# Kernel tuning notes

Hardware: AMD Instinct MI355X
Metric: run time of the kernel (lower is better)

The kernel has to match this reference:

```python
import jax, jax.numpy as jnp
import numpy as np

N, G, K, D = 16, 4096, 8, 2  # agents, grid points (64x64 flattened), fiber dim, manifold dim


def setup_inputs() -> dict:
    key = jax.random.key(0)
    k0, k1, k2, k3 = jax.random.split(key, 4)
    I = jnp.eye(K, dtype=jnp.float32)
    # frames and links: identity + small perturbation (invertible, as init_twist_scale=0.05 implies)
    omega = I + 0.05 * jax.random.normal(k0, (N, G, K, K), dtype=jnp.float32)
    links = I + 0.05 * jax.random.normal(k1, (N, D, G, K, K), dtype=jnp.float32)
    mu_q = jax.random.normal(k2, (N, G, K), dtype=jnp.float32)
    A = 0.3 * jax.random.normal(k3, (N, G, K, K), dtype=jnp.float32)
    sigma_q = A @ A.swapaxes(-1, -2) + I  # SPD covariances
    return {"omega": omega, "links": links, "mu_q": mu_q, "sigma_q": sigma_q}


def reference(omega, links, mu_q, sigma_q):
    """pairwise_alignment_with_twists: E[i,j,g] = KL(q_i || Omega_ij[q_j]).

    full_transport: Omega_ij = omega_i @ V_i @ inv(omega_j),
    V_i = I + sum_d (link_{i,d} - I)   (links depend only on i, per source).
    """
    I = jnp.eye(K, dtype=omega.dtype)
    V = I + jnp.sum(links - I, axis=1)                       # (N,G,K,K)
    T = omega @ V                                            # omega_i V_i, (N,G,K,K)
    omega_inv = jnp.linalg.inv(omega)                        # (N,G,K,K)
    Om = jnp.einsum('igab,jgbc->ijgac', T, omega_inv)        # (N,N,G,K,K)

    mu_t = jnp.einsum('ijgab,jgb->ijga', Om, mu_q)           # transported means
    sig_t = jnp.einsum('ijgab,jgbc,ijgdc->ijgad', Om, sigma_q, Om)  # Om Sigma Om^T

    inv2 = jnp.linalg.inv(sig_t)                             # Sigma2^{-1}
    diff = mu_t - mu_q[:, None]                              # (N,N,G,K)
    tr = jnp.einsum('ijgab,igba->ijg', inv2, sigma_q)        # tr(Sigma2^{-1} Sigma1)
    quad = jnp.einsum('ijga,ijgab,ijgb->ijg', diff, inv2, diff)
    ld2 = jnp.linalg.slogdet(sig_t)[1]                       # (N,N,G)
    ld1 = jnp.linalg.slogdet(sigma_q)[1]                     # (N,G)
    E = 0.5 * (tr + quad - K + ld2 - ld1[:, None, :])
    # zero the diagonal (i == j skipped in the original loop)
    mask = 1.0 - jnp.eye(N, dtype=E.dtype)
    return E * mask[:, :, None]
```

## Files before the change

kernel.cpp:

```cpp
#include <hip/hip_runtime.h>
#include <math.h>

#define NN 16
#define GG 4096
#define GP 2
#define STR 76
#define NWG (GG / GP)

template <int CTRL>
__device__ __forceinline__ float dppf(float x) {
    return __builtin_bit_cast(float, __builtin_amdgcn_mov_dpp(
        __builtin_bit_cast(int, x), CTRL, 0xF, 0xF, true));
}
__device__ __forceinline__ float qb(float x, int L) {
    switch (L) {
        case 0:  return dppf<0x00>(x);
        case 1:  return dppf<0x55>(x);
        case 2:  return dppf<0xAA>(x);
        default: return dppf<0xFF>(x);
    }
}
__device__ __forceinline__ float qsum(float x) {
    x += dppf<0xB1>(x);
    x += dppf<0x4E>(x);
    return x;
}
__device__ __forceinline__ void bcast_row(float out[8], const float r0[8],
                                          const float r1[8], int k) {
#pragma unroll
    for (int c = 0; c < 8; ++c) {
        float s = (k < 4) ? r0[c] : r1[c];
        out[c] = qb(s, k & 3);
    }
}
__device__ __forceinline__ float sel_lo(const float r[8], int q) {
    return (q == 0) ? r[0] : (q == 1) ? r[1] : (q == 2) ? r[2] : r[3];
}
__device__ __forceinline__ float sel_hi(const float r[8], int q) {
    return (q == 0) ? r[4] : (q == 1) ? r[5] : (q == 2) ? r[6] : r[7];
}
__device__ __forceinline__ void ld_row(float r[8], const float* p) {
    float4 x = *(const float4*)p, y = *(const float4*)(p + 4);
    r[0] = x.x; r[1] = x.y; r[2] = x.z; r[3] = x.w;
    r[4] = y.x; r[5] = y.y; r[6] = y.z; r[7] = y.w;
}
__device__ __forceinline__ void st_row(float* p, const float r[8]) {
    *(float4*)p       = make_float4(r[0], r[1], r[2], r[3]);
    *(float4*)(p + 4) = make_float4(r[4], r[5], r[6], r[7]);
}
__device__ __forceinline__ float dot8(const float a[8], const float b[8]) {
    float s = a[0] * b[0];
    s = fmaf(a[1], b[1], s); s = fmaf(a[2], b[2], s);
    s = fmaf(a[3], b[3], s); s = fmaf(a[4], b[4], s);
    s = fmaf(a[5], b[5], s); s = fmaf(a[6], b[6], s);
    s = fmaf(a[7], b[7], s);
    return s;
}

__device__ __forceinline__ float gj4(float r0[8], float r1[8], int q) {
    float pp = 1.0f;
#pragma unroll
    for (int k = 0; k < 8; ++k) {
        float Mk[8];
        bcast_row(Mk, r0, r1, k);
        float p = Mk[k];
        pp *= p;
        float ip = 1.0f / p;
        bool own0 = (k < 4) && (q == k);
        bool own1 = (k >= 4) && (q == k - 4);
        float m0 = -(own0 ? -1.0f : r0[k]) * ip;
        float m1 = -(own1 ? -1.0f : r1[k]) * ip;
#pragma unroll
        for (int c = 0; c < 8; ++c) {
            float b0 = own0 ? 0.0f : r0[c];
            float b1 = own1 ? 0.0f : r1[c];
            r0[c] = fmaf(m0, Mk[c], b0);
            r1[c] = fmaf(m1, Mk[c], b1);
        }
        r0[k] = m0;
        r1[k] = m1;
    }
    return pp;
}

__global__ __launch_bounds__(256) void pairkl_kernel(
    const float* __restrict__ omega, const float* __restrict__ links,
    const float* __restrict__ mu, const float* __restrict__ sigma,
    float* __restrict__ out) {
    __shared__ __align__(16) float sh_x[GP][NN][STR];
    __shared__ __align__(16) float sh_y[GP][NN][STR];

    const int bid  = blockIdx.x;
    const int work = (bid & 7) * (NWG / 8) + (bid >> 3);
    const int g0   = work * GP;
    const int t    = threadIdx.x;
    const int wid  = t >> 6;
    const int gl   = wid & 1;
    const int isB  = wid >> 1;
    const int lane = t & 63;
    const int item = lane >> 2;
    const int q    = lane & 3;
    const int g    = g0 + gl;
    const int mb   = (item * GG + g) * 64;

    if (!isB) {
        float v0[8], v1[8], o0[8], o1[8], s0[8], s1[8], mq[8];
        {
            const float* l0p = links + ((item * 2 + 0) * GG + g) * 64;
            const float* l1p = links + ((item * 2 + 1) * GG + g) * 64;
            float la[8], lb[8];
            ld_row(la, l0p + q * 8);
            ld_row(lb, l1p + q * 8);
#pragma unroll
            for (int c = 0; c < 8; ++c)
                v0[c] = la[c] + lb[c] - ((c == q) ? 1.f : 0.f);
            ld_row(la, l0p + (q + 4) * 8);
            ld_row(lb, l1p + (q + 4) * 8);
#pragma unroll
            for (int c = 0; c < 8; ++c)
                v1[c] = la[c] + lb[c] - ((c == q + 4) ? 1.f : 0.f);
        }
        ld_row(o0, omega + mb + q * 8);
        ld_row(o1, omega + mb + (q + 4) * 8);
        ld_row(s0, sigma + mb + q * 8);
        ld_row(s1, sigma + mb + (q + 4) * 8);
        ld_row(mq, mu + (item * GG + g) * 8);
        float R0[8], R1[8];
#pragma unroll
        for (int c = 0; c < 8; ++c) { R0[c] = 0.f; R1[c] = 0.f; }
#pragma unroll
        for (int b = 0; b < 8; ++b) {
            float Vb[8]; bcast_row(Vb, v0, v1, b);
#pragma unroll
            for (int c = 0; c < 8; ++c) {
                R0[c] = fmaf(o0[b], Vb[c], R0[c]);
                R1[c] = fmaf(o1[b], Vb[c], R1[c]);
            }
        }
        float ldT = logf(fabsf(gj4(R0, R1, q)));
        float Z0[8], Z1[8];
#pragma unroll
        for (int c = 0; c < 8; ++c) { Z0[c] = 0.f; Z1[c] = 0.f; }
#pragma unroll
        for (int b = 0; b < 8; ++b) {
            float Sb[8]; bcast_row(Sb, s0, s1, b);
#pragma unroll
            for (int c = 0; c < 8; ++c) {
                Z0[c] = fmaf(R0[b], Sb[c], Z0[c]);
                Z1[c] = fmaf(R1[b], Sb[c], Z1[c]);
            }
        }
        float u_lo = dot8(R0, mq), u_hi = dot8(R1, mq);
        float uf[8];
#pragma unroll
        for (int c = 0; c < 4; ++c) { uf[c] = qb(u_lo, c); uf[c + 4] = qb(u_hi, c); }
        float X0[8], X1[8];
#pragma unroll
        for (int c = 0; c < 8; ++c) {
            float Wc[8]; bcast_row(Wc, R0, R1, c);
            X0[c] = fmaf(u_lo, uf[c], dot8(Z0, Wc));
            X1[c] = fmaf(u_hi, uf[c], dot8(Z1, Wc));
        }
        st_row(&sh_x[gl][item][q * 8], X0);
        st_row(&sh_x[gl][item][(q + 4) * 8], X1);
        if (q == 0) {
            *(float4*)&sh_x[gl][item][64] = make_float4(uf[0], uf[1], uf[2], uf[3]);
            *(float4*)&sh_x[gl][item][68] = make_float4(uf[4], uf[5], uf[6], uf[7]);
            *(float2*)&sh_x[gl][item][72] = make_float2(2.f * ldT, 1.f);
        }
    } else {
        float o0[8], o1[8], s0[8], s1[8], mq[8];
        ld_row(o0, omega + mb + q * 8);
        ld_row(o1, omega + mb + (q + 4) * 8);
        ld_row(s0, sigma + mb + q * 8);
        ld_row(s1, sigma + mb + (q + 4) * 8);
        ld_row(mq, mu + (item * GG + g) * 8);
        float ld1 = logf(fabsf(gj4(s0, s1, q)));
        float cc  = qsum(dot8(s0, mq) * sel_lo(mq, q) +
                         dot8(s1, mq) * sel_hi(mq, q));
        if (q == 0) *(float2*)&sh_x[gl][item][74] = make_float2(-ld1, 0.f);
        float t10[8], t11[8];
#pragma unroll
        for (int c = 0; c < 8; ++c) { t10[c] = 0.f; t11[c] = 0.f; }
#pragma unroll
        for (int a = 0; a < 8; ++a) {
            float Oa[8]; bcast_row(Oa, o0, o1, a);
            float Sa[8]; bcast_row(Sa, s0, s1, a);
            float oqa = sel_lo(Oa, q), oqa4 = sel_hi(Oa, q);
#pragma unroll
            for (int c = 0; c < 8; ++c) {
                t10[c] = fmaf(oqa,  Sa[c], t10[c]);
                t11[c] = fmaf(oqa4, Sa[c], t11[c]);
            }
        }
        float w_lo = dot8(t10, mq), w_hi = dot8(t11, mq);
        float wf[8];
#pragma unroll
        for (int c = 0; c < 4; ++c) { wf[c] = qb(w_lo, c); wf[c + 4] = qb(w_hi, c); }
        float P0[8], P1[8];
#pragma unroll
        for (int c = 0; c < 8; ++c) { P0[c] = 0.f; P1[c] = 0.f; }
#pragma unroll
        for (int b = 0; b < 8; ++b) {
            float Ob[8]; bcast_row(Ob, o0, o1, b);
#pragma unroll
            for (int c = 0; c < 8; ++c) {
                P0[c] = fmaf(t10[b], Ob[c], P0[c]);
                P1[c] = fmaf(t11[b], Ob[c], P1[c]);
            }
        }
        st_row(&sh_y[gl][item][q * 8], P0);
        st_row(&sh_y[gl][item][(q + 4) * 8], P1);
        float ldo = logf(fabsf(gj4(o0, o1, q)));
        if (q == 0) {
            float s_j = ld1 - 2.f * ldo + cc - 8.0f;
            *(float4*)&sh_y[gl][item][64] =
                make_float4(-2.f * wf[0], -2.f * wf[1], -2.f * wf[2], -2.f * wf[3]);
            *(float4*)&sh_y[gl][item][68] =
                make_float4(-2.f * wf[4], -2.f * wf[5], -2.f * wf[6], -2.f * wf[7]);
            *(float4*)&sh_y[gl][item][72] = make_float4(1.f, s_j, 1.f, 0.f);
        }
    }
    __syncthreads();

    if (t < 128) {
        const int gl2 = t >> 6, r = t & 63;
        const int i0 = r >> 3, j0 = r & 7;
        const int i1 = i0 + 8, j1 = j0 + 8;
        const float4* x0 = (const float4*)&sh_x[gl2][i0][0];
        const float4* x1 = (const float4*)&sh_x[gl2][i1][0];
        const float4* y0 = (const float4*)&sh_y[gl2][j0][0];
        const float4* y1 = (const float4*)&sh_y[gl2][j1][0];
        float d00 = 0.f, d01 = 0.f, d10 = 0.f, d11 = 0.f;
#pragma unroll
        for (int k = 0; k < STR / 4; ++k) {
            float4 a0 = x0[k], a1 = x1[k], b0 = y0[k], b1 = y1[k];
            d00 = fmaf(a0.x, b0.x, d00); d00 = fmaf(a0.y, b0.y, d00);
            d00 = fmaf(a0.z, b0.z, d00); d00 = fmaf(a0.w, b0.w, d00);
            d01 = fmaf(a0.x, b1.x, d01); d01 = fmaf(a0.y, b1.y, d01);
            d01 = fmaf(a0.z, b1.z, d01); d01 = fmaf(a0.w, b1.w, d01);
            d10 = fmaf(a1.x, b0.x, d10); d10 = fmaf(a1.y, b0.y, d10);
            d10 = fmaf(a1.z, b0.z, d10); d10 = fmaf(a1.w, b0.w, d10);
            d11 = fmaf(a1.x, b1.x, d11); d11 = fmaf(a1.y, b1.y, d11);
            d11 = fmaf(a1.z, b1.z, d11); d11 = fmaf(a1.w, b1.w, d11);
        }
        const int gg = g0 + gl2;
        const bool dg = (i0 == j0);
        out[(i0 * NN + j0) * GG + gg] = dg ? 0.f : 0.5f * d00;
        out[(i0 * NN + j1) * GG + gg] = 0.5f * d01;
        out[(i1 * NN + j0) * GG + gg] = 0.5f * d10;
        out[(i1 * NN + j1) * GG + gg] = dg ? 0.f : 0.5f * d11;
    }
}

extern "C" void kernel_launch(void* const* d_in, const int* in_sizes, int n_in,
                              void* d_out, int out_size, void* d_ws, size_t ws_size,
                              hipStream_t stream) {
    const float* omega = (const float*)d_in[0];
    const float* links = (const float*)d_in[1];
    const float* mu    = (const float*)d_in[2];
    const float* sigma = (const float*)d_in[3];
    float* out = (float*)d_out;
    hipLaunchKernelGGL(pairkl_kernel, dim3(NWG), dim3(256), 0, stream,
                       omega, links, mu, sigma, out);
}
```

Before: 26.96 us.

## Collapse to one wave per grid point, removing block barrier

Each grid point is now handled by a single 64-lane wavefront that does both the source-side and target-side work in sequence, instead of four waves split across two grid points and two roles. The __syncthreads is replaced by a compiler memory fence, since LDS exchange stays inside one wave, and the final pairwise dot-product phase uses all lanes instead of half the block. Register arrays are reused to limit pressure. The cost is that each wave now carries twice the serial ALU work and the launch has 4096 small blocks, which cuts per-wave parallelism and adds scheduling overhead.

```diff
diff --git a/kernel.cpp b/kernel.cpp
--- a/kernel.cpp
+++ b/kernel.cpp
@@ -3,9 +3,8 @@
 
 #define NN 16
 #define GG 4096
-#define GP 2
 #define STR 76
-#define NWG (GG / GP)
+#define NWG GG
 
 template <int CTRL>
 __device__ __forceinline__ float dppf(float x) {
@@ -83,48 +82,42 @@
     return pp;
 }
 
-__global__ __launch_bounds__(256) void pairkl_kernel(
+__global__ __launch_bounds__(64) void pairkl_kernel(
     const float* __restrict__ omega, const float* __restrict__ links,
     const float* __restrict__ mu, const float* __restrict__ sigma,
     float* __restrict__ out) {
-    __shared__ __align__(16) float sh_x[GP][NN][STR];
-    __shared__ __align__(16) float sh_y[GP][NN][STR];
+    __shared__ __align__(16) float sh_x[NN][STR];
+    __shared__ __align__(16) float sh_y[NN][STR];
 
     const int bid  = blockIdx.x;
-    const int work = (bid & 7) * (NWG / 8) + (bid >> 3);
-    const int g0   = work * GP;
-    const int t    = threadIdx.x;
-    const int wid  = t >> 6;
-    const int gl   = wid & 1;
-    const int isB  = wid >> 1;
-    const int lane = t & 63;
+    const int g    = (bid & 7) * (NWG / 8) + (bid >> 3);
+    const int lane = threadIdx.x;
     const int item = lane >> 2;
     const int q    = lane & 3;
-    const int g    = g0 + gl;
     const int mb   = (item * GG + g) * 64;
 
-    if (!isB) {
-        float v0[8], v1[8], o0[8], o1[8], s0[8], s1[8], mq[8];
-        {
-            const float* l0p = links + ((item * 2 + 0) * GG + g) * 64;
-            const float* l1p = links + ((item * 2 + 1) * GG + g) * 64;
-            float la[8], lb[8];
-            ld_row(la, l0p + q * 8);
-            ld_row(lb, l1p + q * 8);
-#pragma unroll
-            for (int c = 0; c < 8; ++c)
-                v0[c] = la[c] + lb[c] - ((c == q) ? 1.f : 0.f);
-            ld_row(la, l0p + (q + 4) * 8);
-            ld_row(lb, l1p + (q + 4) * 8);
-#pragma unroll
-            for (int c = 0; c < 8; ++c)
-                v1[c] = la[c] + lb[c] - ((c == q + 4) ? 1.f : 0.f);
-        }
-        ld_row(o0, omega + mb + q * 8);
-        ld_row(o1, omega + mb + (q + 4) * 8);
-        ld_row(s0, sigma + mb + q * 8);
-        ld_row(s1, sigma + mb + (q + 4) * 8);
-        ld_row(mq, mu + (item * GG + g) * 8);
+    float o0[8], o1[8], s0[8], s1[8], v0[8], v1[8], mq[8];
+    {
+        const float* l0p = links + ((item * 2 + 0) * GG + g) * 64;
+        const float* l1p = links + ((item * 2 + 1) * GG + g) * 64;
+        float la[8], lb[8];
+        ld_row(la, l0p + q * 8);
+        ld_row(lb, l1p + q * 8);
+#pragma unroll
+        for (int c = 0; c < 8; ++c) v0[c] = la[c] + lb[c] - ((c == q) ? 1.f : 0.f);
+        ld_row(la, l0p + (q + 4) * 8);
+        ld_row(lb, l1p + (q + 4) * 8);
+#pragma unroll
+        for (int c = 0; c < 8; ++c) v1[c] = la[c] + lb[c] - ((c == q + 4) ? 1.f : 0.f);
+    }
+    ld_row(o0, omega + mb + q * 8);
+    ld_row(o1, omega + mb + (q + 4) * 8);
+    ld_row(s0, sigma + mb + q * 8);
+    ld_row(s1, sigma + mb + (q + 4) * 8);
+    ld_row(mq, mu + (item * GG + g) * 8);
+
+    float ldT, u_lo, u_hi, uf[8];
+    {
         float R0[8], R1[8];
 #pragma unroll
         for (int c = 0; c < 8; ++c) { R0[c] = 0.f; R1[c] = 0.f; }
@@ -137,7 +130,7 @@
                 R1[c] = fmaf(o1[b], Vb[c], R1[c]);
             }
         }
-        float ldT = logf(fabsf(gj4(R0, R1, q)));
+        ldT = logf(fabsf(gj4(R0, R1, q)));
         float Z0[8], Z1[8];
 #pragma unroll
         for (int c = 0; c < 8; ++c) { Z0[c] = 0.f; Z1[c] = 0.f; }
@@ -150,35 +143,24 @@
                 Z1[c] = fmaf(R1[b], Sb[c], Z1[c]);
             }
         }
-        float u_lo = dot8(R0, mq), u_hi = dot8(R1, mq);
-        float uf[8];
+        u_lo = dot8(R0, mq);
+        u_hi = dot8(R1, mq);
 #pragma unroll
         for (int c = 0; c < 4; ++c) { uf[c] = qb(u_lo, c); uf[c + 4] = qb(u_hi, c); }
-        float X0[8], X1[8];
 #pragma unroll
         for (int c = 0; c < 8; ++c) {
             float Wc[8]; bcast_row(Wc, R0, R1, c);
-            X0[c] = fmaf(u_lo, uf[c], dot8(Z0, Wc));
-            X1[c] = fmaf(u_hi, uf[c], dot8(Z1, Wc));
-        }
-        st_row(&sh_x[gl][item][q * 8], X0);
-        st_row(&sh_x[gl][item][(q + 4) * 8], X1);
-        if (q == 0) {
-            *(float4*)&sh_x[gl][item][64] = make_float4(uf[0], uf[1], uf[2], uf[3]);
-            *(float4*)&sh_x[gl][item][68] = make_float4(uf[4], uf[5], uf[6], uf[7]);
-            *(float2*)&sh_x[gl][item][72] = make_float2(2.f * ldT, 1.f);
-        }
-    } else {
-        float o0[8], o1[8], s0[8], s1[8], mq[8];
-        ld_row(o0, omega + mb + q * 8);
-        ld_row(o1, omega + mb + (q + 4) * 8);
-        ld_row(s0, sigma + mb + q * 8);
-        ld_row(s1, sigma + mb + (q + 4) * 8);
-        ld_row(mq, mu + (item * GG + g) * 8);
-        float ld1 = logf(fabsf(gj4(s0, s1, q)));
-        float cc  = qsum(dot8(s0, mq) * sel_lo(mq, q) +
-                         dot8(s1, mq) * sel_hi(mq, q));
-        if (q == 0) *(float2*)&sh_x[gl][item][74] = make_float2(-ld1, 0.f);
+            v0[c] = fmaf(u_lo, uf[c], dot8(Z0, Wc));
+            v1[c] = fmaf(u_hi, uf[c], dot8(Z1, Wc));
+        }
+        st_row(&sh_x[item][q * 8], v0);
+        st_row(&sh_x[item][(q + 4) * 8], v1);
+    }
+
+    float ld1, cc, wf[8];
+    {
+        ld1 = logf(fabsf(gj4(s0, s1, q)));
+        cc  = qsum(dot8(s0, mq) * sel_lo(mq, q) + dot8(s1, mq) * sel_hi(mq, q));
         float t10[8], t11[8];
 #pragma unroll
         for (int c = 0; c < 8; ++c) { t10[c] = 0.f; t11[c] = 0.f; }
@@ -194,43 +176,45 @@
             }
         }
         float w_lo = dot8(t10, mq), w_hi = dot8(t11, mq);
-        float wf[8];
 #pragma unroll
         for (int c = 0; c < 4; ++c) { wf[c] = qb(w_lo, c); wf[c + 4] = qb(w_hi, c); }
-        float P0[8], P1[8];
-#pragma unroll
-        for (int c = 0; c < 8; ++c) { P0[c] = 0.f; P1[c] = 0.f; }
+#pragma unroll
+        for (int c = 0; c < 8; ++c) { s0[c] = 0.f; s1[c] = 0.f; }
 #pragma unroll
         for (int b = 0; b < 8; ++b) {
             float Ob[8]; bcast_row(Ob, o0, o1, b);
 #pragma unroll
             for (int c = 0; c < 8; ++c) {
-                P0[c] = fmaf(t10[b], Ob[c], P0[c]);
-                P1[c] = fmaf(t11[b], Ob[c], P1[c]);
-            }
-        }
-        st_row(&sh_y[gl][item][q * 8], P0);
-        st_row(&sh_y[gl][item][(q + 4) * 8], P1);
-        float ldo = logf(fabsf(gj4(o0, o1, q)));
-        if (q == 0) {
-            float s_j = ld1 - 2.f * ldo + cc - 8.0f;
-            *(float4*)&sh_y[gl][item][64] =
-                make_float4(-2.f * wf[0], -2.f * wf[1], -2.f * wf[2], -2.f * wf[3]);
-            *(float4*)&sh_y[gl][item][68] =
-                make_float4(-2.f * wf[4], -2.f * wf[5], -2.f * wf[6], -2.f * wf[7]);
-            *(float4*)&sh_y[gl][item][72] = make_float4(1.f, s_j, 1.f, 0.f);
-        }
-    }
-    __syncthreads();
-
-    if (t < 128) {
-        const int gl2 = t >> 6, r = t & 63;
-        const int i0 = r >> 3, j0 = r & 7;
+                s0[c] = fmaf(t10[b], Ob[c], s0[c]);
+                s1[c] = fmaf(t11[b], Ob[c], s1[c]);
+            }
+        }
+        st_row(&sh_y[item][q * 8], s0);
+        st_row(&sh_y[item][(q + 4) * 8], s1);
+    }
+    float ldo = logf(fabsf(gj4(o0, o1, q)));
+
+    if (q == 0) {
+        float a_i = 2.f * ldT - ld1;
+        float s_j = ld1 - 2.f * ldo + cc - 8.0f;
+        *(float4*)&sh_x[item][64] = make_float4(uf[0], uf[1], uf[2], uf[3]);
+        *(float4*)&sh_x[item][68] = make_float4(uf[4], uf[5], uf[6], uf[7]);
+        *(float4*)&sh_x[item][72] = make_float4(a_i, 1.f, 0.f, 0.f);
+        *(float4*)&sh_y[item][64] =
+            make_float4(-2.f * wf[0], -2.f * wf[1], -2.f * wf[2], -2.f * wf[3]);
+        *(float4*)&sh_y[item][68] =
+            make_float4(-2.f * wf[4], -2.f * wf[5], -2.f * wf[6], -2.f * wf[7]);
+        *(float4*)&sh_y[item][72] = make_float4(1.f, s_j, 0.f, 0.f);
+    }
+    asm volatile("" ::: "memory");
+
+    {
+        const int i0 = lane >> 3, j0 = lane & 7;
         const int i1 = i0 + 8, j1 = j0 + 8;
-        const float4* x0 = (const float4*)&sh_x[gl2][i0][0];
-        const float4* x1 = (const float4*)&sh_x[gl2][i1][0];
-        const float4* y0 = (const float4*)&sh_y[gl2][j0][0];
-        const float4* y1 = (const float4*)&sh_y[gl2][j1][0];
+        const float4* x0 = (const float4*)&sh_x[i0][0];
+        const float4* x1 = (const float4*)&sh_x[i1][0];
+        const float4* y0 = (const float4*)&sh_y[j0][0];
+        const float4* y1 = (const float4*)&sh_y[j1][0];
         float d00 = 0.f, d01 = 0.f, d10 = 0.f, d11 = 0.f;
 #pragma unroll
         for (int k = 0; k < STR / 4; ++k) {
@@ -244,12 +228,11 @@
             d11 = fmaf(a1.x, b1.x, d11); d11 = fmaf(a1.y, b1.y, d11);
             d11 = fmaf(a1.z, b1.z, d11); d11 = fmaf(a1.w, b1.w, d11);
         }
-        const int gg = g0 + gl2;
         const bool dg = (i0 == j0);
-        out[(i0 * NN + j0) * GG + gg] = dg ? 0.f : 0.5f * d00;
-        out[(i0 * NN + j1) * GG + gg] = 0.5f * d01;
-        out[(i1 * NN + j0) * GG + gg] = 0.5f * d10;
-        out[(i1 * NN + j1) * GG + gg] = dg ? 0.f : 0.5f * d11;
+        out[(i0 * NN + j0) * GG + g] = dg ? 0.f : 0.5f * d00;
+        out[(i0 * NN + j1) * GG + g] = 0.5f * d01;
+        out[(i1 * NN + j0) * GG + g] = 0.5f * d10;
+        out[(i1 * NN + j1) * GG + g] = dg ? 0.f : 0.5f * d11;
     }
 }
 
@@ -261,6 +244,6 @@
     const float* mu    = (const float*)d_in[2];
     const float* sigma = (const float*)d_in[3];
     float* out = (float*)d_out;
-    hipLaunchKernelGGL(pairkl_kernel, dim3(NWG), dim3(256), 0, stream,
+    hipLaunchKernelGGL(pairkl_kernel, dim3(NWG), dim3(64), 0, stream,
                        omega, links, mu, sigma, out);
 }
```

Measured after the change: 26.88 us. Within noise of the previous version (-0.3%).
